# Kernel optimization log

Measured on AMD Instinct MI355X. Metric: run time of the kernel, lower is better.

## Reference

```python
import jax, jax.numpy as jnp
import numpy as np

B = 4096
N_COL = 100      # all-numerical columns
N_COND = 64      # d*m = 4*16
D = 4
TOTAL = N_COL * N_COND   # 6400
N_RODT = TOTAL // D      # 1600
N_EST = 160              # max(2,int(sqrt(100))) * N_COND // D
N_FOREST = 100
N_HIDDEN = 128
N_CLASS = 10
EPS = 1e-5


def group_norm(x, w, b, groups):
    # x: [B, C] (spatial dim of 1 dropped); normalize within each channel group
    Bn, C = x.shape
    xg = x.reshape(Bn, groups, C // groups)
    mu = xg.mean(-1, keepdims=True)
    var = ((xg - mu) ** 2).mean(-1, keepdims=True)
    xn = ((xg - mu) * jax.lax.rsqrt(var + EPS)).reshape(Bn, C)
    return xn * w + b


def layer_norm(x, w, b):
    mu = x.mean(-1, keepdims=True)
    var = ((x - mu) ** 2).mean(-1, keepdims=True)
    return (x - mu) * jax.lax.rsqrt(var + EPS) * w + b


def setup_inputs() -> dict:
    key = jax.random.key(0)
    ks = jax.random.split(key, 16)
    s = 0.3  # weight scale
    x = jax.random.normal(ks[0], (B, N_COL), jnp.float32)
    w1 = jax.random.normal(ks[1], (N_COL, N_COND), jnp.float32) * s
    b1 = jax.random.normal(ks[2], (N_COL, N_COND), jnp.float32) * s
    perm = jax.random.permutation(ks[3], TOTAL)
    gn1_w = jnp.ones((TOTAL,), jnp.float32)
    gn1_b = jnp.zeros((TOTAL,), jnp.float32)
    conv2_w = jax.random.normal(ks[4], (N_RODT, D, D), jnp.float32) * s
    conv2_b = jax.random.normal(ks[5], (TOTAL,), jnp.float32) * s
    gn2_w = jnp.ones((TOTAL,), jnp.float32)
    gn2_b = jnp.zeros((TOTAL,), jnp.float32)
    conv3_w = jax.random.normal(ks[6], (N_RODT, D, 1), jnp.float32) * s
    conv3_b = jax.random.normal(ks[7], (N_RODT,), jnp.float32) * s
    # sample-without-replacement per forest (eval-mode fixed indices)
    swr = jax.vmap(lambda k: jax.random.permutation(k, N_RODT)[:N_EST])(
        jax.random.split(ks[8], N_FOREST))
    E = jax.random.normal(ks[9], (N_RODT, N_HIDDEN), jnp.float32)
    ln1_w = jnp.ones((N_HIDDEN,), jnp.float32)
    ln1_b = jnp.zeros((N_HIDDEN,), jnp.float32)
    fc1_w = jax.random.normal(ks[10], (N_HIDDEN, N_HIDDEN), jnp.float32) * (1.0 / np.sqrt(N_HIDDEN))
    fc1_b = jnp.zeros((N_HIDDEN,), jnp.float32)
    ln2_w = jnp.ones((N_HIDDEN,), jnp.float32)
    ln2_b = jnp.zeros((N_HIDDEN,), jnp.float32)
    fc2_w = jax.random.normal(ks[11], (N_HIDDEN, N_CLASS), jnp.float32) * (1.0 / np.sqrt(N_HIDDEN))
    fc2_b = jnp.zeros((N_CLASS,), jnp.float32)
    return dict(x=x, w1=w1, b1=b1, perm=perm, gn1_w=gn1_w, gn1_b=gn1_b,
                conv2_w=conv2_w, conv2_b=conv2_b, gn2_w=gn2_w, gn2_b=gn2_b,
                conv3_w=conv3_w, conv3_b=conv3_b, swr=swr, E=E,
                ln1_w=ln1_w, ln1_b=ln1_b, fc1_w=fc1_w, fc1_b=fc1_b,
                ln2_w=ln2_w, ln2_b=ln2_b, fc2_w=fc2_w, fc2_b=fc2_b)


def reference(x, w1, b1, perm, gn1_w, gn1_b, conv2_w, conv2_b, gn2_w, gn2_b,
              conv3_w, conv3_b, swr, E, ln1_w, ln1_b, fc1_w, fc1_b,
              ln2_w, ln2_b, fc2_w, fc2_b):
    b = x.shape[0]
    # --- ConditionGeneration (numerical path): per-column 1->n_cond group conv + sigmoid
    M = jax.nn.sigmoid(x[:, :, None] * w1[None] + b1[None])        # [B, n_col, n_cond]
    M = M.transpose(0, 2, 1)                                        # [B, n_cond, n_col]
    # --- rODTConstruction: flatten + fixed permutation
    O = M.reshape(b, -1)[:, perm]                                   # [B, total]
    # --- phi_2: GN -> grouped 4->4 conv -> ReLU -> GN -> grouped 4->1 conv
    h = group_norm(O, gn1_w, gn1_b, N_RODT)
    h = jnp.einsum('bgi,gio->bgo', h.reshape(b, N_RODT, D), conv2_w).reshape(b, TOTAL) + conv2_b
    h = jax.nn.relu(h)
    h = group_norm(h, gn2_w, gn2_b, N_RODT)
    w = jnp.einsum('bgi,gio->bgo', h.reshape(b, N_RODT, D), conv3_w)[..., 0] + conv3_b  # [B, n_rodt] (n_head=1)
    # --- rODT forest: gather estimators, softmax over estimators, weighted sum of rODT embeddings
    ws = jax.nn.softmax(w[:, swr], axis=2)                          # [B, n_forest, n_est]
    Ep = E[swr]                                                     # [n_forest, n_est, n_hidden]
    F = jnp.einsum('bfe,fed->bfd', ws, Ep)                          # [B, n_forest, n_hidden]
    # --- bagging MLP (dropout=0)
    h2 = layer_norm(F, ln1_w, ln1_b)
    h2 = jax.nn.relu(h2 @ fc1_w + fc1_b)
    h2 = layer_norm(h2, ln2_w, ln2_b)
    y_hat = h2 @ fc2_w + fc2_b                                      # [B, n_forest, n_class]
    return y_hat.mean(1)                                            # [B, n_class]
```

## Files before the change

kernel.cpp:

```cpp
#include <hip/hip_runtime.h>
#include <hip/hip_bf16.h>
#include <stdint.h>

#define NB 4096
#define NCOL 100
#define NCOND 64
#define NTOTAL 6400
#define NRODT 1600
#define NEST 160
#define NFOR 100
#define NHID 128
#define NCLS 10
#define GEPS 1e-5f

typedef __attribute__((ext_vector_type(8))) short short8;
typedef __attribute__((ext_vector_type(4))) float floatx4;

__device__ __forceinline__ unsigned f2bfu(float x) {
  union { float f; unsigned u; } v; v.f = x;
  return (v.u + 0x8000u) >> 16;
}

__global__ __launch_bounds__(256) void k1_w(
    const float* __restrict__ x, const float* __restrict__ w1,
    const float* __restrict__ b1, const int* __restrict__ perm,
    const float* __restrict__ gn1w, const float* __restrict__ gn1b,
    const float* __restrict__ c2w, const float* __restrict__ c2b,
    const float* __restrict__ gn2w, const float* __restrict__ gn2b,
    const float* __restrict__ c3w, const float* __restrict__ c3b,
    float* __restrict__ wT)
{
  __shared__ float xl[64 * NCOL];
  const int b0 = blockIdx.x * 64;
  const int g  = blockIdx.y * 64 + (threadIdx.x >> 2);
  const int i4 = threadIdx.x & 3;
  for (int i = threadIdx.x; i < 64 * NCOL; i += 256)
    xl[i] = x[(size_t)b0 * NCOL + i];
  __syncthreads();

  const int4 p4 = *(const int4*)(perm + 4 * g);
  const int pv[4] = {p4.x, p4.y, p4.z, p4.w};
  float w1v[4], b1v[4];
  int pc[4];
#pragma unroll
  for (int i = 0; i < 4; i++) {
    unsigned p = (unsigned)pv[i];
    unsigned j = p / 100u;
    unsigned cc = p - j * 100u;
    pc[i] = (int)cc;
    w1v[i] = w1[cc * NCOND + j];
    b1v[i] = b1[cc * NCOND + j];
  }
  const float4 g1w = *(const float4*)(gn1w + 4 * g);
  const float4 g1b = *(const float4*)(gn1b + 4 * g);
  const float4 cw0 = *(const float4*)(c2w + 16 * g);
  const float4 cw1 = *(const float4*)(c2w + 16 * g + 4);
  const float4 cw2 = *(const float4*)(c2w + 16 * g + 8);
  const float4 cw3 = *(const float4*)(c2w + 16 * g + 12);
  const float4 cbv = *(const float4*)(c2b + 4 * g);
  const float4 g2w = *(const float4*)(gn2w + 4 * g);
  const float4 g2b = *(const float4*)(gn2b + 4 * g);
  const float4 c3v = *(const float4*)(c3w + 4 * g);
  const float c3bv = c3b[g];

  for (int k = 0; k < 4; k++) {
    float v4[4];
#pragma unroll
    for (int j = 0; j < 4; j++) {
      const int bb = k * 16 + i4 * 4 + j;
      float O[4];
#pragma unroll
      for (int i = 0; i < 4; i++) {
        float a = xl[bb * NCOL + pc[i]] * w1v[i] + b1v[i];
        O[i] = 1.0f / (1.0f + __expf(-a));
      }
      float mu = 0.25f * (O[0] + O[1] + O[2] + O[3]);
      float d[4], var = 0.f;
#pragma unroll
      for (int i = 0; i < 4; i++) { d[i] = O[i] - mu; var += d[i] * d[i]; }
      float rs = rsqrtf(0.25f * var + GEPS);
      float xn0 = d[0] * rs * g1w.x + g1b.x;
      float xn1 = d[1] * rs * g1w.y + g1b.y;
      float xn2 = d[2] * rs * g1w.z + g1b.z;
      float xn3 = d[3] * rs * g1w.w + g1b.w;
      float h[4];
      h[0] = xn0*cw0.x + xn1*cw1.x + xn2*cw2.x + xn3*cw3.x + cbv.x;
      h[1] = xn0*cw0.y + xn1*cw1.y + xn2*cw2.y + xn3*cw3.y + cbv.y;
      h[2] = xn0*cw0.z + xn1*cw1.z + xn2*cw2.z + xn3*cw3.z + cbv.z;
      h[3] = xn0*cw0.w + xn1*cw1.w + xn2*cw2.w + xn3*cw3.w + cbv.w;
#pragma unroll
      for (int i = 0; i < 4; i++) h[i] = fmaxf(h[i], 0.f);
      float mu2 = 0.25f * (h[0] + h[1] + h[2] + h[3]);
      float e[4], var2 = 0.f;
#pragma unroll
      for (int i = 0; i < 4; i++) { e[i] = h[i] - mu2; var2 += e[i] * e[i]; }
      float rs2 = rsqrtf(0.25f * var2 + GEPS);
      float hn0 = e[0] * rs2 * g2w.x + g2b.x;
      float hn1 = e[1] * rs2 * g2w.y + g2b.y;
      float hn2 = e[2] * rs2 * g2w.z + g2b.z;
      float hn3 = e[3] * rs2 * g2w.w + g2b.w;
      v4[j] = hn0*c3v.x + hn1*c3v.y + hn2*c3v.z + hn3*c3v.w + c3bv;
    }
    *(float4*)(wT + (size_t)g * NB + b0 + k * 16 + i4 * 4) =
        make_float4(v4[0], v4[1], v4[2], v4[3]);
  }
}

__global__ __launch_bounds__(256) void k0_prep(
    const float* __restrict__ E, const int* __restrict__ swr,
    const float* __restrict__ fc1w, const float* __restrict__ fc2w,
    unsigned short* __restrict__ Bf, unsigned short* __restrict__ W1f,
    unsigned short* __restrict__ W2f)
{
  __shared__ int ridx[NEST];
  const int tid = threadIdx.x;
  const int blk = blockIdx.x;

  if (blk < NFOR) {
    if (tid < NEST) ridx[tid] = swr[blk * NEST + tid];
    __syncthreads();
    for (int m = tid; m < 2560; m += 256) {
      int lane = m & 63, rest = m >> 6;
      int kc = rest % 5, n = rest / 5;
      int q = lane >> 4, c = lane & 15;
      int e0 = kc * 32 + q * 8;
      int h = n * 16 + c;
      union { unsigned short v[8]; uint4 u; } t;
#pragma unroll
      for (int j = 0; j < 8; j++)
        t.v[j] = (unsigned short)f2bfu(E[(size_t)ridx[e0 + j] * NHID + h]);
      *(uint4*)(Bf + (size_t)blk * 20480 + (size_t)m * 8) = t.u;
    }
  } else if (blk == NFOR) {
    for (int m = tid; m < 2048; m += 256) {
      int lane = m & 63, rest = m >> 6;
      int kc = rest & 3, n = rest >> 2;
      int q = lane >> 4, c = lane & 15;
      int k0 = kc * 32 + q * 8;
      int o = n * 16 + c;
      union { unsigned short v[8]; uint4 u; } t;
#pragma unroll
      for (int j = 0; j < 8; j++)
        t.v[j] = (unsigned short)f2bfu(fc1w[(size_t)(k0 + j) * NHID + o]);
      *(uint4*)(W1f + (size_t)m * 8) = t.u;
    }
  } else {
    for (int m = tid; m < 256; m += 256) {
      int lane = m & 63, kc = m >> 6;
      int q = lane >> 4, c = lane & 15;
      int k0 = kc * 32 + q * 8;
      union { unsigned short v[8]; uint4 u; } t;
#pragma unroll
      for (int j = 0; j < 8; j++)
        t.v[j] = (unsigned short)f2bfu(c < NCLS ? fc2w[(size_t)(k0 + j) * NCLS + c] : 0.f);
      *(uint4*)(W2f + (size_t)m * 8) = t.u;
    }
  }
}

__global__ __launch_bounds__(256, 4) void k3_mfma(
    const float* __restrict__ wT,
    const int* __restrict__ swr,
    const unsigned short* __restrict__ Bf,
    const unsigned short* __restrict__ W1f,
    const unsigned short* __restrict__ W2f,
    const float* __restrict__ ln1w, const float* __restrict__ ln1b,
    const float* __restrict__ fc1b,
    const float* __restrict__ ln2w, const float* __restrict__ ln2b,
    const float* __restrict__ fc2b,
    float* __restrict__ out)
{
  __shared__ unsigned short lsA[64 * 168];
  __shared__ int ridx[NEST];

  const int tid = threadIdx.x;
  const int b0 = blockIdx.x * 64;
  const int f  = blockIdx.y;
  const int lane = tid & 63, wv = tid >> 6;
  const int c = lane & 15, q = lane >> 4;

  if (tid < NEST) ridx[tid] = swr[f * NEST + tid];
  __syncthreads();

  const int r = tid >> 2, ch = tid & 3;
  const float* wcol = wT + b0 + r;
  const int* rp = ridx + ch * 40;
  float g[40];
#pragma unroll
  for (int j = 0; j < 40; j++)
    g[j] = wcol[(size_t)rp[j] * NB];

  float mx = -1e30f;
#pragma unroll
  for (int j = 0; j < 40; j++) mx = fmaxf(mx, g[j]);
  mx = fmaxf(mx, __shfl_xor(mx, 1));
  mx = fmaxf(mx, __shfl_xor(mx, 2));
  float s = 0.f;
#pragma unroll
  for (int j = 0; j < 40; j++) { g[j] = __expf(g[j] - mx); s += g[j]; }
  s += __shfl_xor(s, 1);
  s += __shfl_xor(s, 2);
  const float inv = 1.0f / s;

  unsigned* dst = (unsigned*)(lsA + r * 168) + ch * 20;
#pragma unroll
  for (int k = 0; k < 20; k++) {
    unsigned u0 = f2bfu(g[2 * k] * inv);
    unsigned u1 = f2bfu(g[2 * k + 1] * inv);
    dst[k] = u0 | (u1 << 16);
  }

  const unsigned short* pa = lsA + (wv * 16 + c) * 168 + q * 8;
  short8 a1[5];
#pragma unroll
  for (int kc = 0; kc < 5; kc++) a1[kc] = *(const short8*)(pa + kc * 32);

  floatx4 acc[8];
#pragma unroll
  for (int n = 0; n < 8; n++) acc[n] = (floatx4){0.f, 0.f, 0.f, 0.f};

  const unsigned short* bbase = Bf + (size_t)f * 20480 + lane * 8;
#pragma unroll
  for (int n = 0; n < 8; n++) {
    const unsigned short* bp = bbase + n * 2560;
#pragma unroll
    for (int kc = 0; kc < 5; kc++) {
      short8 b = *(const short8*)(bp + kc * 512);
      acc[n] = __builtin_amdgcn_mfma_f32_16x16x32_bf16(a1[kc], b, acc[n], 0, 0, 0);
    }
  }

  {
    float lw[8], lb[8];
#pragma unroll
    for (int n = 0; n < 8; n++) { lw[n] = ln1w[n * 16 + c]; lb[n] = ln1b[n * 16 + c]; }
#pragma unroll
    for (int rr = 0; rr < 4; rr++) {
      float s1 = 0.f, s2 = 0.f;
#pragma unroll
      for (int n = 0; n < 8; n++) { float v = acc[n][rr]; s1 += v; s2 += v * v; }
#pragma unroll
      for (int off = 1; off < 16; off <<= 1) {
        s1 += __shfl_xor(s1, off); s2 += __shfl_xor(s2, off);
      }
      float mu = s1 * (1.f / 128.f);
      float var = fmaxf(s2 * (1.f / 128.f) - mu * mu, 0.f);
      float rs = rsqrtf(var + GEPS);
#pragma unroll
      for (int n = 0; n < 8; n++)
        acc[n][rr] = (acc[n][rr] - mu) * rs * lw[n] + lb[n];
    }
  }

#pragma unroll
  for (int rr = 0; rr < 4; rr++)
#pragma unroll
    for (int n = 0; n < 8; n++)
      lsA[(wv * 16 + q * 4 + rr) * 168 + n * 16 + c] =
          (unsigned short)f2bfu(acc[n][rr]);

  short8 a2[4];
#pragma unroll
  for (int kc = 0; kc < 4; kc++) a2[kc] = *(const short8*)(pa + kc * 32);
#pragma unroll
  for (int n = 0; n < 8; n++) acc[n] = (floatx4){0.f, 0.f, 0.f, 0.f};
  const unsigned short* w1p = W1f + lane * 8;
#pragma unroll
  for (int n = 0; n < 8; n++) {
#pragma unroll
    for (int kc = 0; kc < 4; kc++) {
      short8 b = *(const short8*)(w1p + (n * 4 + kc) * 512);
      acc[n] = __builtin_amdgcn_mfma_f32_16x16x32_bf16(a2[kc], b, acc[n], 0, 0, 0);
    }
  }

  {
    float fb[8], lw[8], lb[8];
#pragma unroll
    for (int n = 0; n < 8; n++) {
      fb[n] = fc1b[n * 16 + c];
      lw[n] = ln2w[n * 16 + c]; lb[n] = ln2b[n * 16 + c];
    }
#pragma unroll
    for (int rr = 0; rr < 4; rr++) {
#pragma unroll
      for (int n = 0; n < 8; n++) acc[n][rr] = fmaxf(acc[n][rr] + fb[n], 0.f);
      float s1 = 0.f, s2 = 0.f;
#pragma unroll
      for (int n = 0; n < 8; n++) { float v = acc[n][rr]; s1 += v; s2 += v * v; }
#pragma unroll
      for (int off = 1; off < 16; off <<= 1) {
        s1 += __shfl_xor(s1, off); s2 += __shfl_xor(s2, off);
      }
      float mu = s1 * (1.f / 128.f);
      float var = fmaxf(s2 * (1.f / 128.f) - mu * mu, 0.f);
      float rs = rsqrtf(var + GEPS);
#pragma unroll
      for (int n = 0; n < 8; n++)
        acc[n][rr] = (acc[n][rr] - mu) * rs * lw[n] + lb[n];
    }
  }

#pragma unroll
  for (int rr = 0; rr < 4; rr++)
#pragma unroll
    for (int n = 0; n < 8; n++)
      lsA[(wv * 16 + q * 4 + rr) * 168 + n * 16 + c] =
          (unsigned short)f2bfu(acc[n][rr]);

  short8 a3[4];
#pragma unroll
  for (int kc = 0; kc < 4; kc++) a3[kc] = *(const short8*)(pa + kc * 32);
  floatx4 o4 = (floatx4){0.f, 0.f, 0.f, 0.f};
#pragma unroll
  for (int kc = 0; kc < 4; kc++) {
    short8 b = *(const short8*)(W2f + kc * 512 + lane * 8);
    o4 = __builtin_amdgcn_mfma_f32_16x16x32_bf16(a3[kc], b, o4, 0, 0, 0);
  }
  if (c < NCLS) {
    float bias = fc2b[c];
#pragma unroll
    for (int rr = 0; rr < 4; rr++)
      atomicAdd(out + (size_t)(b0 + wv * 16 + q * 4 + rr) * NCLS + c,
                (o4[rr] + bias) * 0.01f);
  }
}

extern "C" void kernel_launch(void* const* d_in, const int* in_sizes, int n_in,
                              void* d_out, int out_size, void* d_ws, size_t ws_size,
                              hipStream_t stream)
{
  (void)in_sizes; (void)n_in; (void)ws_size;
  const float* x    = (const float*)d_in[0];
  const float* w1   = (const float*)d_in[1];
  const float* b1   = (const float*)d_in[2];
  const int*   perm = (const int*)d_in[3];
  const float* gn1w = (const float*)d_in[4];
  const float* gn1b = (const float*)d_in[5];
  const float* c2w  = (const float*)d_in[6];
  const float* c2b  = (const float*)d_in[7];
  const float* gn2w = (const float*)d_in[8];
  const float* gn2b = (const float*)d_in[9];
  const float* c3w  = (const float*)d_in[10];
  const float* c3b  = (const float*)d_in[11];
  const int*   swr  = (const int*)d_in[12];
  const float* E    = (const float*)d_in[13];
  const float* ln1w = (const float*)d_in[14];
  const float* ln1b = (const float*)d_in[15];
  const float* fc1w = (const float*)d_in[16];
  const float* fc1b = (const float*)d_in[17];
  const float* ln2w = (const float*)d_in[18];
  const float* ln2b = (const float*)d_in[19];
  const float* fc2w = (const float*)d_in[20];
  const float* fc2b = (const float*)d_in[21];
  float* out = (float*)d_out;

  const size_t W_BYTES = (size_t)NB * NRODT * 4;
  float* wTbuf = (float*)d_ws;
  unsigned short* Bfb   = (unsigned short*)((char*)d_ws + W_BYTES);
  unsigned short* W1fb  = (unsigned short*)((char*)d_ws + W_BYTES + 4096000);
  unsigned short* W2fb  = (unsigned short*)((char*)d_ws + W_BYTES + 4096000 + 32768);

  hipMemsetAsync(d_out, 0, (size_t)out_size * sizeof(float), stream);
  dim3 g1(NB / 64, NRODT / 64);
  k1_w<<<g1, 256, 0, stream>>>(x, w1, b1, perm, gn1w, gn1b, c2w, c2b,
                               gn2w, gn2b, c3w, c3b, wTbuf);
  k0_prep<<<NFOR + 2, 256, 0, stream>>>(E, swr, fc1w, fc2w, Bfb, W1fb, W2fb);
  dim3 g3(NB / 64, NFOR);
  k3_mfma<<<g3, 256, 0, stream>>>(wTbuf, swr, Bfb, W1fb, W2fb,
                                  ln1w, ln1b, fc1b, ln2w, ln2b, fc2b, out);
}
```

Baseline: 255.8 us.

## Merge prep kernels and output zeroing into one launch, raise MFMA occupancy

Folds the rODT weight kernel, the bf16 repacking of E/fc1/fc2 and the output zeroing into a single heterogeneous launch, so one kernel launch and the memset disappear. The MFMA kernel now streams A fragments per k-chunk instead of holding them all in registers, and raises its launch_bounds minimum occupancy from 4 to 6 blocks. The register cap may cause spills. The merged prep blocks also add some branch divergence across block types.

```diff
diff --git a/kernel.cpp b/kernel.cpp
--- a/kernel.cpp
+++ b/kernel.cpp
@@ -21,103 +21,101 @@
   return (v.u + 0x8000u) >> 16;
 }
 
-__global__ __launch_bounds__(256) void k1_w(
+__global__ __launch_bounds__(256) void k01_prep(
     const float* __restrict__ x, const float* __restrict__ w1,
     const float* __restrict__ b1, const int* __restrict__ perm,
     const float* __restrict__ gn1w, const float* __restrict__ gn1b,
     const float* __restrict__ c2w, const float* __restrict__ c2b,
     const float* __restrict__ gn2w, const float* __restrict__ gn2b,
     const float* __restrict__ c3w, const float* __restrict__ c3b,
-    float* __restrict__ wT)
+    const float* __restrict__ E, const int* __restrict__ swr,
+    const float* __restrict__ fc1w, const float* __restrict__ fc2w,
+    float* __restrict__ wT,
+    unsigned short* __restrict__ Bf, unsigned short* __restrict__ W1f,
+    unsigned short* __restrict__ W2f, float* __restrict__ out)
 {
   __shared__ float xl[64 * NCOL];
-  const int b0 = blockIdx.x * 64;
-  const int g  = blockIdx.y * 64 + (threadIdx.x >> 2);
-  const int i4 = threadIdx.x & 3;
-  for (int i = threadIdx.x; i < 64 * NCOL; i += 256)
-    xl[i] = x[(size_t)b0 * NCOL + i];
-  __syncthreads();
-
-  const int4 p4 = *(const int4*)(perm + 4 * g);
-  const int pv[4] = {p4.x, p4.y, p4.z, p4.w};
-  float w1v[4], b1v[4];
-  int pc[4];
-#pragma unroll
-  for (int i = 0; i < 4; i++) {
-    unsigned p = (unsigned)pv[i];
-    unsigned j = p / 100u;
-    unsigned cc = p - j * 100u;
-    pc[i] = (int)cc;
-    w1v[i] = w1[cc * NCOND + j];
-    b1v[i] = b1[cc * NCOND + j];
-  }
-  const float4 g1w = *(const float4*)(gn1w + 4 * g);
-  const float4 g1b = *(const float4*)(gn1b + 4 * g);
-  const float4 cw0 = *(const float4*)(c2w + 16 * g);
-  const float4 cw1 = *(const float4*)(c2w + 16 * g + 4);
-  const float4 cw2 = *(const float4*)(c2w + 16 * g + 8);
-  const float4 cw3 = *(const float4*)(c2w + 16 * g + 12);
-  const float4 cbv = *(const float4*)(c2b + 4 * g);
-  const float4 g2w = *(const float4*)(gn2w + 4 * g);
-  const float4 g2b = *(const float4*)(gn2b + 4 * g);
-  const float4 c3v = *(const float4*)(c3w + 4 * g);
-  const float c3bv = c3b[g];
-
-  for (int k = 0; k < 4; k++) {
-    float v4[4];
-#pragma unroll
-    for (int j = 0; j < 4; j++) {
-      const int bb = k * 16 + i4 * 4 + j;
-      float O[4];
-#pragma unroll
-      for (int i = 0; i < 4; i++) {
-        float a = xl[bb * NCOL + pc[i]] * w1v[i] + b1v[i];
-        O[i] = 1.0f / (1.0f + __expf(-a));
-      }
-      float mu = 0.25f * (O[0] + O[1] + O[2] + O[3]);
-      float d[4], var = 0.f;
-#pragma unroll
-      for (int i = 0; i < 4; i++) { d[i] = O[i] - mu; var += d[i] * d[i]; }
-      float rs = rsqrtf(0.25f * var + GEPS);
-      float xn0 = d[0] * rs * g1w.x + g1b.x;
-      float xn1 = d[1] * rs * g1w.y + g1b.y;
-      float xn2 = d[2] * rs * g1w.z + g1b.z;
-      float xn3 = d[3] * rs * g1w.w + g1b.w;
-      float h[4];
-      h[0] = xn0*cw0.x + xn1*cw1.x + xn2*cw2.x + xn3*cw3.x + cbv.x;
-      h[1] = xn0*cw0.y + xn1*cw1.y + xn2*cw2.y + xn3*cw3.y + cbv.y;
-      h[2] = xn0*cw0.z + xn1*cw1.z + xn2*cw2.z + xn3*cw3.z + cbv.z;
-      h[3] = xn0*cw0.w + xn1*cw1.w + xn2*cw2.w + xn3*cw3.w + cbv.w;
-#pragma unroll
-      for (int i = 0; i < 4; i++) h[i] = fmaxf(h[i], 0.f);
-      float mu2 = 0.25f * (h[0] + h[1] + h[2] + h[3]);
-      float e[4], var2 = 0.f;
-#pragma unroll
-      for (int i = 0; i < 4; i++) { e[i] = h[i] - mu2; var2 += e[i] * e[i]; }
-      float rs2 = rsqrtf(0.25f * var2 + GEPS);
-      float hn0 = e[0] * rs2 * g2w.x + g2b.x;
-      float hn1 = e[1] * rs2 * g2w.y + g2b.y;
-      float hn2 = e[2] * rs2 * g2w.z + g2b.z;
-      float hn3 = e[3] * rs2 * g2w.w + g2b.w;
-      v4[j] = hn0*c3v.x + hn1*c3v.y + hn2*c3v.z + hn3*c3v.w + c3bv;
-    }
-    *(float4*)(wT + (size_t)g * NB + b0 + k * 16 + i4 * 4) =
-        make_float4(v4[0], v4[1], v4[2], v4[3]);
-  }
-}
-
-__global__ __launch_bounds__(256) void k0_prep(
-    const float* __restrict__ E, const int* __restrict__ swr,
-    const float* __restrict__ fc1w, const float* __restrict__ fc2w,
-    unsigned short* __restrict__ Bf, unsigned short* __restrict__ W1f,
-    unsigned short* __restrict__ W2f)
-{
   __shared__ int ridx[NEST];
   const int tid = threadIdx.x;
   const int blk = blockIdx.x;
 
-  if (blk < NFOR) {
-    if (tid < NEST) ridx[tid] = swr[blk * NEST + tid];
+  if (blk < 1600) {
+    const int b0 = (blk & 63) * 64;
+    const int g  = (blk >> 6) * 64 + (tid >> 2);
+    const int i4 = tid & 3;
+    for (int i = tid; i < 64 * NCOL; i += 256)
+      xl[i] = x[(size_t)b0 * NCOL + i];
+    __syncthreads();
+
+    const int4 p4 = *(const int4*)(perm + 4 * g);
+    const int pv[4] = {p4.x, p4.y, p4.z, p4.w};
+    float w1v[4], b1v[4];
+    int pc[4];
+#pragma unroll
+    for (int i = 0; i < 4; i++) {
+      unsigned p = (unsigned)pv[i];
+      unsigned j = p / 100u;
+      unsigned cc = p - j * 100u;
+      pc[i] = (int)cc;
+      w1v[i] = w1[cc * NCOND + j];
+      b1v[i] = b1[cc * NCOND + j];
+    }
+    const float4 g1w = *(const float4*)(gn1w + 4 * g);
+    const float4 g1b = *(const float4*)(gn1b + 4 * g);
+    const float4 cw0 = *(const float4*)(c2w + 16 * g);
+    const float4 cw1 = *(const float4*)(c2w + 16 * g + 4);
+    const float4 cw2 = *(const float4*)(c2w + 16 * g + 8);
+    const float4 cw3 = *(const float4*)(c2w + 16 * g + 12);
+    const float4 cbv = *(const float4*)(c2b + 4 * g);
+    const float4 g2w = *(const float4*)(gn2w + 4 * g);
+    const float4 g2b = *(const float4*)(gn2b + 4 * g);
+    const float4 c3v = *(const float4*)(c3w + 4 * g);
+    const float c3bv = c3b[g];
+
+    for (int k = 0; k < 4; k++) {
+      float v4[4];
+#pragma unroll
+      for (int j = 0; j < 4; j++) {
+        const int bb = k * 16 + i4 * 4 + j;
+        float O[4];
+#pragma unroll
+        for (int i = 0; i < 4; i++) {
+          float a = xl[bb * NCOL + pc[i]] * w1v[i] + b1v[i];
+          O[i] = 1.0f / (1.0f + __expf(-a));
+        }
+        float mu = 0.25f * (O[0] + O[1] + O[2] + O[3]);
+        float d[4], var = 0.f;
+#pragma unroll
+        for (int i = 0; i < 4; i++) { d[i] = O[i] - mu; var += d[i] * d[i]; }
+        float rs = rsqrtf(0.25f * var + GEPS);
+        float xn0 = d[0] * rs * g1w.x + g1b.x;
+        float xn1 = d[1] * rs * g1w.y + g1b.y;
+        float xn2 = d[2] * rs * g1w.z + g1b.z;
+        float xn3 = d[3] * rs * g1w.w + g1b.w;
+        float h[4];
+        h[0] = xn0*cw0.x + xn1*cw1.x + xn2*cw2.x + xn3*cw3.x + cbv.x;
+        h[1] = xn0*cw0.y + xn1*cw1.y + xn2*cw2.y + xn3*cw3.y + cbv.y;
+        h[2] = xn0*cw0.z + xn1*cw1.z + xn2*cw2.z + xn3*cw3.z + cbv.z;
+        h[3] = xn0*cw0.w + xn1*cw1.w + xn2*cw2.w + xn3*cw3.w + cbv.w;
+#pragma unroll
+        for (int i = 0; i < 4; i++) h[i] = fmaxf(h[i], 0.f);
+        float mu2 = 0.25f * (h[0] + h[1] + h[2] + h[3]);
+        float e[4], var2 = 0.f;
+#pragma unroll
+        for (int i = 0; i < 4; i++) { e[i] = h[i] - mu2; var2 += e[i] * e[i]; }
+        float rs2 = rsqrtf(0.25f * var2 + GEPS);
+        float hn0 = e[0] * rs2 * g2w.x + g2b.x;
+        float hn1 = e[1] * rs2 * g2w.y + g2b.y;
+        float hn2 = e[2] * rs2 * g2w.z + g2b.z;
+        float hn3 = e[3] * rs2 * g2w.w + g2b.w;
+        v4[j] = hn0*c3v.x + hn1*c3v.y + hn2*c3v.z + hn3*c3v.w + c3bv;
+      }
+      *(float4*)(wT + (size_t)g * NB + b0 + k * 16 + i4 * 4) =
+          make_float4(v4[0], v4[1], v4[2], v4[3]);
+    }
+  } else if (blk < 1600 + NFOR) {
+    const int fblk = blk - 1600;
+    if (tid < NEST) ridx[tid] = swr[fblk * NEST + tid];
     __syncthreads();
     for (int m = tid; m < 2560; m += 256) {
       int lane = m & 63, rest = m >> 6;
@@ -129,9 +127,9 @@
 #pragma unroll
       for (int j = 0; j < 8; j++)
         t.v[j] = (unsigned short)f2bfu(E[(size_t)ridx[e0 + j] * NHID + h]);
-      *(uint4*)(Bf + (size_t)blk * 20480 + (size_t)m * 8) = t.u;
-    }
-  } else if (blk == NFOR) {
+      *(uint4*)(Bf + (size_t)fblk * 20480 + (size_t)m * 8) = t.u;
+    }
+  } else if (blk == 1600 + NFOR) {
     for (int m = tid; m < 2048; m += 256) {
       int lane = m & 63, rest = m >> 6;
       int kc = rest & 3, n = rest >> 2;
@@ -144,7 +142,7 @@
         t.v[j] = (unsigned short)f2bfu(fc1w[(size_t)(k0 + j) * NHID + o]);
       *(uint4*)(W1f + (size_t)m * 8) = t.u;
     }
-  } else {
+  } else if (blk == 1601 + NFOR) {
     for (int m = tid; m < 256; m += 256) {
       int lane = m & 63, kc = m >> 6;
       int q = lane >> 4, c = lane & 15;
@@ -155,10 +153,15 @@
         t.v[j] = (unsigned short)f2bfu(c < NCLS ? fc2w[(size_t)(k0 + j) * NCLS + c] : 0.f);
       *(uint4*)(W2f + (size_t)m * 8) = t.u;
     }
+  } else {
+    const int z = blk - (1602 + NFOR);
+    float4 zz = make_float4(0.f, 0.f, 0.f, 0.f);
+    for (int i = z * 256 + tid; i < NB * NCLS / 4; i += 3 * 256)
+      ((float4*)out)[i] = zz;
   }
 }
 
-__global__ __launch_bounds__(256, 4) void k3_mfma(
+__global__ __launch_bounds__(256, 6) void k3_mfma(
     const float* __restrict__ wT,
     const int* __restrict__ swr,
     const unsigned short* __restrict__ Bf,
@@ -211,22 +214,18 @@
   }
 
   const unsigned short* pa = lsA + (wv * 16 + c) * 168 + q * 8;
-  short8 a1[5];
-#pragma unroll
-  for (int kc = 0; kc < 5; kc++) a1[kc] = *(const short8*)(pa + kc * 32);
-
   floatx4 acc[8];
 #pragma unroll
   for (int n = 0; n < 8; n++) acc[n] = (floatx4){0.f, 0.f, 0.f, 0.f};
 
   const unsigned short* bbase = Bf + (size_t)f * 20480 + lane * 8;
 #pragma unroll
-  for (int n = 0; n < 8; n++) {
-    const unsigned short* bp = bbase + n * 2560;
-#pragma unroll
-    for (int kc = 0; kc < 5; kc++) {
-      short8 b = *(const short8*)(bp + kc * 512);
-      acc[n] = __builtin_amdgcn_mfma_f32_16x16x32_bf16(a1[kc], b, acc[n], 0, 0, 0);
+  for (int kc = 0; kc < 5; kc++) {
+    short8 a = *(const short8*)(pa + kc * 32);
+#pragma unroll
+    for (int n = 0; n < 8; n++) {
+      short8 b = *(const short8*)(bbase + n * 2560 + kc * 512);
+      acc[n] = __builtin_amdgcn_mfma_f32_16x16x32_bf16(a, b, acc[n], 0, 0, 0);
     }
   }
 
@@ -259,18 +258,21 @@
       lsA[(wv * 16 + q * 4 + rr) * 168 + n * 16 + c] =
           (unsigned short)f2bfu(acc[n][rr]);
 
-  short8 a2[4];
-#pragma unroll
-  for (int kc = 0; kc < 4; kc++) a2[kc] = *(const short8*)(pa + kc * 32);
-#pragma unroll
-  for (int n = 0; n < 8; n++) acc[n] = (floatx4){0.f, 0.f, 0.f, 0.f};
-  const unsigned short* w1p = W1f + lane * 8;
-#pragma unroll
-  for (int n = 0; n < 8; n++) {
-#pragma unroll
-    for (int kc = 0; kc < 4; kc++) {
-      short8 b = *(const short8*)(w1p + (n * 4 + kc) * 512);
-      acc[n] = __builtin_amdgcn_mfma_f32_16x16x32_bf16(a2[kc], b, acc[n], 0, 0, 0);
+  {
+    short8 a0 = *(const short8*)(pa);
+    short8 a1 = *(const short8*)(pa + 32);
+    short8 a2 = *(const short8*)(pa + 64);
+    short8 a3 = *(const short8*)(pa + 96);
+#pragma unroll
+    for (int n = 0; n < 8; n++) acc[n] = (floatx4){0.f, 0.f, 0.f, 0.f};
+    const unsigned short* w1p = W1f + lane * 8;
+#pragma unroll
+    for (int n = 0; n < 8; n++) {
+      const unsigned short* wp = w1p + n * 2048;
+      acc[n] = __builtin_amdgcn_mfma_f32_16x16x32_bf16(a0, *(const short8*)(wp),        acc[n], 0, 0, 0);
+      acc[n] = __builtin_amdgcn_mfma_f32_16x16x32_bf16(a1, *(const short8*)(wp + 512),  acc[n], 0, 0, 0);
+      acc[n] = __builtin_amdgcn_mfma_f32_16x16x32_bf16(a2, *(const short8*)(wp + 1024), acc[n], 0, 0, 0);
+      acc[n] = __builtin_amdgcn_mfma_f32_16x16x32_bf16(a3, *(const short8*)(wp + 1536), acc[n], 0, 0, 0);
     }
   }
 
@@ -308,14 +310,12 @@
       lsA[(wv * 16 + q * 4 + rr) * 168 + n * 16 + c] =
           (unsigned short)f2bfu(acc[n][rr]);
 
-  short8 a3[4];
-#pragma unroll
-  for (int kc = 0; kc < 4; kc++) a3[kc] = *(const short8*)(pa + kc * 32);
   floatx4 o4 = (floatx4){0.f, 0.f, 0.f, 0.f};
 #pragma unroll
   for (int kc = 0; kc < 4; kc++) {
+    short8 a = *(const short8*)(pa + kc * 32);
     short8 b = *(const short8*)(W2f + kc * 512 + lane * 8);
-    o4 = __builtin_amdgcn_mfma_f32_16x16x32_bf16(a3[kc], b, o4, 0, 0, 0);
+    o4 = __builtin_amdgcn_mfma_f32_16x16x32_bf16(a, b, o4, 0, 0, 0);
   }
   if (c < NCLS) {
     float bias = fc2b[c];
@@ -330,7 +330,7 @@
                               void* d_out, int out_size, void* d_ws, size_t ws_size,
                               hipStream_t stream)
 {
-  (void)in_sizes; (void)n_in; (void)ws_size;
+  (void)in_sizes; (void)n_in; (void)ws_size; (void)out_size;
   const float* x    = (const float*)d_in[0];
   const float* w1   = (const float*)d_in[1];
   const float* b1   = (const float*)d_in[2];
@@ -361,11 +361,9 @@
   unsigned short* W1fb  = (unsigned short*)((char*)d_ws + W_BYTES + 4096000);
   unsigned short* W2fb  = (unsigned short*)((char*)d_ws + W_BYTES + 4096000 + 32768);
 
-  hipMemsetAsync(d_out, 0, (size_t)out_size * sizeof(float), stream);
-  dim3 g1(NB / 64, NRODT / 64);
-  k1_w<<<g1, 256, 0, stream>>>(x, w1, b1, perm, gn1w, gn1b, c2w, c2b,
-                               gn2w, gn2b, c3w, c3b, wTbuf);
-  k0_prep<<<NFOR + 2, 256, 0, stream>>>(E, swr, fc1w, fc2w, Bfb, W1fb, W2fb);
+  k01_prep<<<1600 + NFOR + 2 + 3, 256, 0, stream>>>(
+      x, w1, b1, perm, gn1w, gn1b, c2w, c2b, gn2w, gn2b, c3w, c3b,
+      E, swr, fc1w, fc2w, wTbuf, Bfb, W1fb, W2fb, out);
   dim3 g3(NB / 64, NFOR);
   k3_mfma<<<g3, 256, 0, stream>>>(wTbuf, swr, Bfb, W1fb, W2fb,
                                   ln1w, ln1b, fc1b, ln2w, ln2b, fc2b, out);
```

After: 248.1 us. 3.0% less time.
